# Performance work log

Measured on AMD Instinct MI355X. Metric: run time of the kernel, lower is better.

The kernel has to match this reference:

```python
import jax, jax.numpy as jnp
import numpy as np

IDIM = 256
N_UNITS = 512
N_LAYERS = 4
E_UNITS = 2048
H = 8
D_K = N_UNITS // H
EPS = 1e-5


def _layer_norm(x, g, b):
    mu = jnp.mean(x, axis=-1, keepdims=True)
    var = jnp.mean(jnp.square(x - mu), axis=-1, keepdims=True)
    return (x - mu) * jax.lax.rsqrt(var + EPS) * g + b


def setup_inputs() -> dict:
    key = jax.random.key(0)
    ks = jax.random.split(key, 16)
    s = 0.02
    inp = {
        'x': jax.random.normal(ks[0], (4, 2, 1024, IDIM), dtype=jnp.float32),
        'Win': jax.random.normal(ks[1], (N_UNITS, IDIM), dtype=jnp.float32) * s,
        'bin_': jnp.zeros((N_UNITS,), jnp.float32),
        'ln1_g': jnp.ones((N_LAYERS, N_UNITS), jnp.float32),
        'ln1_b': jnp.zeros((N_LAYERS, N_UNITS), jnp.float32),
        'Wq': jax.random.normal(ks[2], (N_LAYERS, N_UNITS, N_UNITS), dtype=jnp.float32) * s,
        'bq': jnp.zeros((N_LAYERS, N_UNITS), jnp.float32),
        'Wk': jax.random.normal(ks[3], (N_LAYERS, N_UNITS, N_UNITS), dtype=jnp.float32) * s,
        'bk': jnp.zeros((N_LAYERS, N_UNITS), jnp.float32),
        'Wv': jax.random.normal(ks[4], (N_LAYERS, N_UNITS, N_UNITS), dtype=jnp.float32) * s,
        'bv': jnp.zeros((N_LAYERS, N_UNITS), jnp.float32),
        'Wo': jax.random.normal(ks[5], (N_LAYERS, N_UNITS, N_UNITS), dtype=jnp.float32) * s,
        'bo': jnp.zeros((N_LAYERS, N_UNITS), jnp.float32),
        'ln2_g': jnp.ones((N_LAYERS, N_UNITS), jnp.float32),
        'ln2_b': jnp.zeros((N_LAYERS, N_UNITS), jnp.float32),
        'W1': jax.random.normal(ks[6], (N_LAYERS, E_UNITS, N_UNITS), dtype=jnp.float32) * s,
        'b1': jnp.zeros((N_LAYERS, E_UNITS), jnp.float32),
        'W2': jax.random.normal(ks[7], (N_LAYERS, N_UNITS, E_UNITS), dtype=jnp.float32) * s,
        'b2': jnp.zeros((N_LAYERS, N_UNITS), jnp.float32),
        'lno_g': jnp.ones((N_UNITS,), jnp.float32),
        'lno_b': jnp.zeros((N_UNITS,), jnp.float32),
    }
    return inp


def reference(x, Win, bin_, ln1_g, ln1_b, Wq, bq, Wk, bk, Wv, bv, Wo, bo,
              ln2_g, ln2_b, W1, b1, W2, b2, lno_g, lno_b):
    bs, num, T, dim = x.shape
    B = bs * num
    # input projection; e is kept as [B*T, n_units] like the torch code
    e = x.reshape(B * T, dim) @ Win.T + bin_
    scale = 1.0 / np.sqrt(D_K).astype(np.float32)
    for i in range(N_LAYERS):
        e = _layer_norm(e, ln1_g[i], ln1_b[i])
        # multi-head self-attention (dropout is identity in eval)
        q = (e @ Wq[i].T + bq[i]).reshape(B, T, H, D_K)
        k = (e @ Wk[i].T + bk[i]).reshape(B, T, H, D_K)
        v = (e @ Wv[i].T + bv[i]).reshape(B, T, H, D_K)
        scores = jnp.einsum('bthd,bshd->bhts', q, k) * scale  # [B,H,T,T]
        att = jax.nn.softmax(scores, axis=-1)
        ctx = jnp.einsum('bhts,bshd->bthd', att, v).reshape(B * T, N_UNITS)
        s = ctx @ Wo[i].T + bo[i]
        e = e + s
        e = _layer_norm(e, ln2_g[i], ln2_b[i])
        # position-wise feed-forward
        hdn = jnp.maximum(e @ W1[i].T + b1[i], 0.0)
        e = e + (hdn @ W2[i].T + b2[i])
    out = _layer_norm(e, lno_g, lno_b)
    return out.reshape(bs, num, T, N_UNITS)
```

## Files before the change

### kernel.cpp

```cpp
#include <hip/hip_runtime.h>
#include <hip/hip_bf16.h>
#include <math.h>
#include <stdint.h>

#define IDIM   256
#define NU     512
#define NL     4
#define EU     2048
#define NH     8
#define DK     64
#define TT     1024
#define NB     8
#define MTOT   8192

typedef short  bf16x8 __attribute__((ext_vector_type(8)));
typedef float  f32x4  __attribute__((ext_vector_type(4)));
typedef unsigned short ushortv2 __attribute__((ext_vector_type(2)));

__device__ __forceinline__ unsigned short f2b(float x) {
  unsigned int u = __float_as_uint(x);
  u += 0x7fffu + ((u >> 16) & 1u);
  return (unsigned short)(u >> 16);
}

__device__ __forceinline__ void gload16(const unsigned short* g, unsigned short* l) {
  auto gp = reinterpret_cast<const __attribute__((address_space(1))) unsigned int*>(
      reinterpret_cast<uintptr_t>(g));
  auto lp = reinterpret_cast<__attribute__((address_space(3))) unsigned int*>(
      reinterpret_cast<uintptr_t>(l));
  __builtin_amdgcn_global_load_lds(gp, lp, 16, 0, 0);
}

__global__ __launch_bounds__(256) void cvt_bf16(
    const float* __restrict__ src, unsigned short* __restrict__ dst, int n) {
  int i = (blockIdx.x * 256 + threadIdx.x) * 8;
  if (i >= n) return;
  float4 a = *(const float4*)(src + i);
  float4 b = *(const float4*)(src + i + 4);
  bf16x8 r;
  r[0] = (short)f2b(a.x); r[1] = (short)f2b(a.y);
  r[2] = (short)f2b(a.z); r[3] = (short)f2b(a.w);
  r[4] = (short)f2b(b.x); r[5] = (short)f2b(b.y);
  r[6] = (short)f2b(b.z); r[7] = (short)f2b(b.w);
  *(bf16x8*)(dst + i) = r;
}

#define GEMM_STAGE(BUF, KK)                                                  \
  _Pragma("unroll") for (int ii = 0; ii < 2; ++ii) {                         \
    gload16(ag + (size_t)(ii * 64) * kdim + (KK), &As[BUF][ii * 2048 + wv * 512]); \
    gload16(bg + (size_t)(ii * 64) * kdim + (KK), &Bs[BUF][ii * 2048 + wv * 512]); \
  }

#define GEMM_CORE(K_, KBEG, KEND)                                            \
  __shared__ unsigned short As[2][128 * 32];                                 \
  __shared__ unsigned short Bs[2][128 * 32];                                 \
  const int kdim = (K_);                                                     \
  const int tid  = threadIdx.x;                                              \
  const int lane = tid & 63;                                                 \
  const int wv   = tid >> 6;                                                 \
  const int wm   = (wv >> 1) * 64;                                           \
  const int wn   = (wv & 1) * 64;                                            \
  const int fr   = lane & 15;                                                \
  const int fc   = lane >> 4;                                                \
  const int srow = wv * 16 + (lane >> 2);                                    \
  const int skk  = (lane & 3) * 8;                                           \
  const unsigned short* ag = A + (size_t)(m0 + srow) * kdim + skk;           \
  const unsigned short* bg = W + (size_t)(n0 + srow) * kdim + skk;           \
  f32x4 acc[4][4];                                                           \
  _Pragma("unroll") for (int i = 0; i < 4; ++i)                              \
    _Pragma("unroll") for (int j = 0; j < 4; ++j)                            \
      acc[i][j] = (f32x4){0.f, 0.f, 0.f, 0.f};                               \
  int cur = 0;                                                               \
  GEMM_STAGE(0, (KBEG))                                                      \
  for (int k0 = (KBEG); k0 < (KEND); k0 += 32) {                             \
    __syncthreads();   \
    if (k0 + 32 < (KEND)) { GEMM_STAGE(cur ^ 1, k0 + 32) }                   \
    const unsigned short* acu = As[cur];                                     \
    const unsigned short* bcu = Bs[cur];                                     \
    bf16x8 af[4], bfr[4];                                                    \
    _Pragma("unroll") for (int mi = 0; mi < 4; ++mi)                         \
      af[mi] = *(const bf16x8*)&acu[(wm + mi * 16 + fr) * 32 + fc * 8];      \
    _Pragma("unroll") for (int ni = 0; ni < 4; ++ni)                         \
      bfr[ni] = *(const bf16x8*)&bcu[(wn + ni * 16 + fr) * 32 + fc * 8];     \
    _Pragma("unroll") for (int mi = 0; mi < 4; ++mi)                         \
      _Pragma("unroll") for (int ni = 0; ni < 4; ++ni)                       \
        acc[mi][ni] = __builtin_amdgcn_mfma_f32_16x16x32_bf16(               \
            af[mi], bfr[ni], acc[mi][ni], 0, 0, 0);                          \
    cur ^= 1;                                                                \
  }

template<int MODE, bool RELU>
__global__ __launch_bounds__(256) void gemm_bf(
    const unsigned short* __restrict__ A, const unsigned short* __restrict__ W,
    const float* __restrict__ bias, float* __restrict__ Cf,
    unsigned short* __restrict__ Cb, int M, int N, int K, int kchunk) {
  const int m0 = blockIdx.y * 128;
  const int n0 = blockIdx.x * 128;
  const int kbeg = blockIdx.z * kchunk;
  const int kend = kbeg + kchunk;
  GEMM_CORE(K, kbeg, kend)

  const bool addb = (blockIdx.z == 0);
#pragma unroll
  for (int ni = 0; ni < 4; ++ni) {
    const int col = n0 + wn + ni * 16 + fr;
    const float bb = (MODE != 2 || addb) ? bias[col] : 0.f;
#pragma unroll
    for (int mi = 0; mi < 4; ++mi) {
      const int row = m0 + wm + mi * 16 + fc * 4;
#pragma unroll
      for (int j = 0; j < 4; ++j) {
        size_t off = (size_t)(row + j) * N + col;
        float r = acc[mi][ni][j] + bb;
        if (RELU) r = fmaxf(r, 0.f);
        if (MODE == 0) Cf[off] = r;
        else if (MODE == 1) Cb[off] = f2b(r);
        else atomicAdd(&Cf[off], r);
      }
    }
  }
}

__global__ __launch_bounds__(256) void gemm_qkv(
    const unsigned short* __restrict__ A,
    const unsigned short* __restrict__ Wq, const unsigned short* __restrict__ Wk,
    const unsigned short* __restrict__ Wv,
    const float* __restrict__ bq, const float* __restrict__ bk,
    const float* __restrict__ bv,
    unsigned short* __restrict__ Oq, unsigned short* __restrict__ Ok,
    unsigned short* __restrict__ Ov) {
  const int zz = blockIdx.z;
  const unsigned short* W  = zz == 0 ? Wq : (zz == 1 ? Wk : Wv);
  const float* bias        = zz == 0 ? bq : (zz == 1 ? bk : bv);
  unsigned short* C        = zz == 0 ? Oq : (zz == 1 ? Ok : Ov);
  const float scale        = zz == 0 ? 0.125f : 1.0f;
  const int m0 = blockIdx.y * 128;
  const int n0 = blockIdx.x * 128;
  GEMM_CORE(NU, 0, NU)

#pragma unroll
  for (int ni = 0; ni < 4; ++ni) {
    const int col = n0 + wn + ni * 16 + fr;
    const float bb = bias[col];
#pragma unroll
    for (int mi = 0; mi < 4; ++mi) {
      const int row = m0 + wm + mi * 16 + fc * 4;
#pragma unroll
      for (int j = 0; j < 4; ++j)
        C[(size_t)(row + j) * NU + col] = f2b((acc[mi][ni][j] + bb) * scale);
    }
  }
}

template<bool WB>
__global__ __launch_bounds__(256) void layernorm_inplace(
    float* __restrict__ e, const float* __restrict__ g,
    const float* __restrict__ b, unsigned short* __restrict__ eb) {
  const int row = blockIdx.x;
  float* x = e + (size_t)row * NU;
  const int tid = threadIdx.x;

  float2 v = *(const float2*)&x[tid * 2];
  float sum = v.x + v.y;
  float sq  = v.x * v.x + v.y * v.y;
#pragma unroll
  for (int o = 32; o > 0; o >>= 1) {
    sum += __shfl_down(sum, o);
    sq  += __shfl_down(sq, o);
  }
  __shared__ float ps[4], pq[4], stat[2];
  const int wid = tid >> 6, lane = tid & 63;
  if (lane == 0) { ps[wid] = sum; pq[wid] = sq; }
  __syncthreads();
  if (tid == 0) {
    float s = ps[0] + ps[1] + ps[2] + ps[3];
    float q = pq[0] + pq[1] + pq[2] + pq[3];
    float mu = s * (1.0f / NU);
    float var = q * (1.0f / NU) - mu * mu;
    stat[0] = mu;
    stat[1] = rsqrtf(var + 1e-5f);
  }
  __syncthreads();
  const float mu = stat[0], rstd = stat[1];
  const float2 gg = *(const float2*)&g[tid * 2];
  const float2 bb = *(const float2*)&b[tid * 2];
  v.x = (v.x - mu) * rstd * gg.x + bb.x;
  v.y = (v.y - mu) * rstd * gg.y + bb.y;
  *(float2*)&x[tid * 2] = v;
  if (WB) {
    ushortv2 o = {f2b(v.x), f2b(v.y)};
    *(ushortv2*)&eb[(size_t)row * NU + tid * 2] = o;
  }
}

__global__ __launch_bounds__(256) void flash_attn_mfma(
    const unsigned short* __restrict__ Q, const unsigned short* __restrict__ K,
    const unsigned short* __restrict__ V, unsigned short* __restrict__ O) {
  constexpr int LSTR = 72;
  constexpr int VSTR = 66;
  __shared__ unsigned short Ks[64 * LSTR];
  __shared__ unsigned short Vt[64 * VSTR];
  __shared__ unsigned short Ps[64 * LSTR];

  const int b = blockIdx.z, h = blockIdx.y;
  const int q0 = blockIdx.x * 64;
  const int tid = threadIdx.x;
  const int lane = tid & 63;
  const int w = tid >> 6;
  const int fr = lane & 15;
  const int fc = lane >> 4;

  const size_t hb = ((size_t)b * TT) * NU + h * DK;

  bf16x8 qf[2];
#pragma unroll
  for (int kc = 0; kc < 2; ++kc)
    qf[kc] = *(const bf16x8*)(Q + hb +
        (size_t)(q0 + w * 16 + fr) * NU + kc * 32 + fc * 8);

  f32x4 ctx[4];
#pragma unroll
  for (int ni = 0; ni < 4; ++ni) ctx[ni] = (f32x4){0.f, 0.f, 0.f, 0.f};
  float m_run[4], l_run[4];
#pragma unroll
  for (int j = 0; j < 4; ++j) { m_run[j] = -1e30f; l_run[j] = 0.f; }

  const int sr = tid >> 2;
  const int sd = (tid & 3) * 16;

  for (int kt = 0; kt < TT; kt += 64) {
    const unsigned short* kp = K + hb + (size_t)(kt + sr) * NU + sd;
    const unsigned short* vp = V + hb + (size_t)(kt + sr) * NU + sd;
    bf16x8 k0 = *(const bf16x8*)kp, k1 = *(const bf16x8*)(kp + 8);
    bf16x8 v0 = *(const bf16x8*)vp, v1 = *(const bf16x8*)(vp + 8);

    __syncthreads();
    *(bf16x8*)&Ks[sr * LSTR + sd]     = k0;
    *(bf16x8*)&Ks[sr * LSTR + sd + 8] = k1;
#pragma unroll
    for (int t = 0; t < 8; ++t) {
      Vt[(sd + t)     * VSTR + sr] = (unsigned short)v0[t];
      Vt[(sd + t + 8) * VSTR + sr] = (unsigned short)v1[t];
    }
    __syncthreads();

    bf16x8 kf[4][2];
#pragma unroll
    for (int ni = 0; ni < 4; ++ni)
#pragma unroll
      for (int kc = 0; kc < 2; ++kc)
        kf[ni][kc] = *(const bf16x8*)&Ks[(ni * 16 + fr) * LSTR + kc * 32 + fc * 8];

    f32x4 sacc[4];
#pragma unroll
    for (int ni = 0; ni < 4; ++ni) sacc[ni] = (f32x4){0.f, 0.f, 0.f, 0.f};
#pragma unroll
    for (int kc = 0; kc < 2; ++kc)
#pragma unroll
      for (int ni = 0; ni < 4; ++ni)
        sacc[ni] = __builtin_amdgcn_mfma_f32_16x16x32_bf16(
            qf[kc], kf[ni][kc], sacc[ni], 0, 0, 0);

    float cm[4];
#pragma unroll
    for (int j = 0; j < 4; ++j)
      cm[j] = fmaxf(fmaxf(sacc[0][j], sacc[1][j]),
                    fmaxf(sacc[2][j], sacc[3][j]));
#pragma unroll
    for (int mask = 1; mask < 16; mask <<= 1)
#pragma unroll
      for (int j = 0; j < 4; ++j)
        cm[j] = fmaxf(cm[j], __shfl_xor(cm[j], mask));

    int need = (cm[0] > m_run[0] + 8.f) | (cm[1] > m_run[1] + 8.f) |
               (cm[2] > m_run[2] + 8.f) | (cm[3] > m_run[3] + 8.f);
    if (__any(need)) {
#pragma unroll
      for (int j = 0; j < 4; ++j) {
        float mn = fmaxf(m_run[j], cm[j]);
        float corr = __expf(m_run[j] - mn);
        m_run[j] = mn;
        l_run[j] *= corr;
#pragma unroll
        for (int ni = 0; ni < 4; ++ni) ctx[ni][j] *= corr;
      }
    }
#pragma unroll
    for (int j = 0; j < 4; ++j)
#pragma unroll
      for (int ni = 0; ni < 4; ++ni) {
        float p = __expf(sacc[ni][j] - m_run[j]);
        l_run[j] += p;
        Ps[(w * 16 + fc * 4 + j) * LSTR + ni * 16 + fr] = f2b(p);
      }

    bf16x8 pf[2], vf[4][2];
#pragma unroll
    for (int kc = 0; kc < 2; ++kc)
      pf[kc] = *(const bf16x8*)&Ps[(w * 16 + fr) * LSTR + kc * 32 + fc * 8];
#pragma unroll
    for (int ni = 0; ni < 4; ++ni)
#pragma unroll
      for (int kc = 0; kc < 2; ++kc)
        vf[ni][kc] = *(const bf16x8*)&Vt[(ni * 16 + fr) * VSTR + kc * 32 + fc * 8];
#pragma unroll
    for (int kc = 0; kc < 2; ++kc)
#pragma unroll
      for (int ni = 0; ni < 4; ++ni)
        ctx[ni] = __builtin_amdgcn_mfma_f32_16x16x32_bf16(
            pf[kc], vf[ni][kc], ctx[ni], 0, 0, 0);
  }

#pragma unroll
  for (int j = 0; j < 4; ++j) {
    float l = l_run[j];
#pragma unroll
    for (int mask = 1; mask < 16; mask <<= 1)
      l += __shfl_xor(l, mask);
    const float inv = 1.0f / l;
    const int row = q0 + w * 16 + fc * 4 + j;
    unsigned short* dst = O + hb + (size_t)row * NU;
#pragma unroll
    for (int ni = 0; ni < 4; ++ni)
      dst[ni * 16 + fr] = f2b(ctx[ni][j] * inv);
  }
}

extern "C" void kernel_launch(void* const* d_in, const int* in_sizes, int n_in,
                              void* d_out, int out_size, void* d_ws, size_t ws_size,
                              hipStream_t stream) {
  const float* x     = (const float*)d_in[0];
  const float* Win   = (const float*)d_in[1];
  const float* bin_  = (const float*)d_in[2];
  const float* ln1_g = (const float*)d_in[3];
  const float* ln1_b = (const float*)d_in[4];
  const float* Wq    = (const float*)d_in[5];
  const float* bq    = (const float*)d_in[6];
  const float* Wk    = (const float*)d_in[7];
  const float* bk    = (const float*)d_in[8];
  const float* Wv    = (const float*)d_in[9];
  const float* bv    = (const float*)d_in[10];
  const float* Wo    = (const float*)d_in[11];
  const float* bo    = (const float*)d_in[12];
  const float* ln2_g = (const float*)d_in[13];
  const float* ln2_b = (const float*)d_in[14];
  const float* W1    = (const float*)d_in[15];
  const float* b1    = (const float*)d_in[16];
  const float* W2    = (const float*)d_in[17];
  const float* b2    = (const float*)d_in[18];
  const float* lno_g = (const float*)d_in[19];
  const float* lno_b = (const float*)d_in[20];

  float* e = (float*)d_out;
  unsigned short* wsb = (unsigned short*)d_ws;
  const size_t M1 = 1u << 20;
  unsigned short* q    = wsb;
  unsigned short* k    = wsb + 4 * M1;
  unsigned short* v    = wsb + 8 * M1;
  unsigned short* ctx  = wsb + 12 * M1;
  unsigned short* hdn  = wsb;
  unsigned short* xbf  = wsb + 4 * M1;
  unsigned short* winb = wsb + 6 * M1;
  unsigned short* ebf  = wsb + 16 * M1;
  unsigned short* wqb  = wsb + 20 * M1;
  unsigned short* wkb  = wsb + 21 * M1;
  unsigned short* wvb  = wsb + 22 * M1;
  unsigned short* wob  = wsb + 23 * M1;
  unsigned short* w1b  = wsb + 24 * M1;
  unsigned short* w2b  = wsb + 28 * M1;

  const dim3 blk(256);
  cvt_bf16<<<1024, blk, 0, stream>>>(x,   xbf,  MTOT * IDIM);
  cvt_bf16<<<64,   blk, 0, stream>>>(Win, winb, NU * IDIM);
  cvt_bf16<<<512,  blk, 0, stream>>>(Wq,  wqb,  NL * NU * NU);
  cvt_bf16<<<512,  blk, 0, stream>>>(Wk,  wkb,  NL * NU * NU);
  cvt_bf16<<<512,  blk, 0, stream>>>(Wv,  wvb,  NL * NU * NU);
  cvt_bf16<<<512,  blk, 0, stream>>>(Wo,  wob,  NL * NU * NU);
  cvt_bf16<<<2048, blk, 0, stream>>>(W1,  w1b,  NL * EU * NU);
  cvt_bf16<<<2048, blk, 0, stream>>>(W2,  w2b,  NL * NU * EU);

  const dim3 gProjIn(NU / 128, MTOT / 128);
  const dim3 gQKV(NU / 128, MTOT / 128, 3);
  const dim3 gWo(NU / 128, MTOT / 128, 4);
  const dim3 gF1(EU / 128, MTOT / 128);
  const dim3 gF2(NU / 128, MTOT / 128, 4);
  const dim3 gAttn(TT / 64, NH, NB);

  gemm_bf<0, false><<<gProjIn, blk, 0, stream>>>(
      xbf, winb, bin_, e, nullptr, MTOT, NU, IDIM, IDIM);

  for (int i = 0; i < NL; ++i) {
    layernorm_inplace<true><<<MTOT, blk, 0, stream>>>(e, ln1_g + i * NU, ln1_b + i * NU, ebf);

    gemm_qkv<<<gQKV, blk, 0, stream>>>(ebf, wqb + (size_t)i * NU * NU,
                                       wkb + (size_t)i * NU * NU,
                                       wvb + (size_t)i * NU * NU,
                                       bq + i * NU, bk + i * NU, bv + i * NU,
                                       q, k, v);

    flash_attn_mfma<<<gAttn, blk, 0, stream>>>(q, k, v, ctx);

    gemm_bf<2, false><<<gWo, blk, 0, stream>>>(
        ctx, wob + (size_t)i * NU * NU, bo + i * NU, e, nullptr,
        MTOT, NU, NU, NU / 4);

    layernorm_inplace<true><<<MTOT, blk, 0, stream>>>(e, ln2_g + i * NU, ln2_b + i * NU, ebf);

    gemm_bf<1, true><<<gF1, blk, 0, stream>>>(
        ebf, w1b + (size_t)i * EU * NU, b1 + i * EU, nullptr, hdn,
        MTOT, EU, NU, NU);

    gemm_bf<2, false><<<gF2, blk, 0, stream>>>(
        hdn, w2b + (size_t)i * NU * EU, b2 + i * NU, e, nullptr,
        MTOT, NU, EU, EU / 4);
  }

  layernorm_inplace<false><<<MTOT, blk, 0, stream>>>(e, lno_g, lno_b, nullptr);
}
```

Baseline: 1.212 ms.

## Transpose V in QKV epilogue, register-staged GEMM loads, wave-per-row layernorm, fused conversion

Several changes land at once. The QKV kernel now writes V pre-transposed, so flash attention loads V tiles with vector stores instead of scattered transposes into shared memory. The GEMM core replaces async global-to-LDS double buffering with register prefetch into a single padded LDS tile, which adds a second barrier per k-step. Layernorm uses one wave per row with no shared-memory reduction, the eight conversion launches become one kernel, and the split-K factor for Wo and FFN2 drops from 4 to 2, which means fewer atomics but less parallelism.

Result: faster. 982.6 us (-18.9%).

```diff
diff --git a/kernel.cpp b/kernel.cpp
--- a/kernel.cpp
+++ b/kernel.cpp
@@ -15,7 +15,8 @@
 
 typedef short  bf16x8 __attribute__((ext_vector_type(8)));
 typedef float  f32x4  __attribute__((ext_vector_type(4)));
-typedef unsigned short ushortv2 __attribute__((ext_vector_type(2)));
+typedef unsigned short ushort4v __attribute__((ext_vector_type(4)));
+typedef unsigned short ushort8v __attribute__((ext_vector_type(8)));
 
 __device__ __forceinline__ unsigned short f2b(float x) {
   unsigned int u = __float_as_uint(x);
@@ -23,37 +24,36 @@
   return (unsigned short)(u >> 16);
 }
 
-__device__ __forceinline__ void gload16(const unsigned short* g, unsigned short* l) {
-  auto gp = reinterpret_cast<const __attribute__((address_space(1))) unsigned int*>(
-      reinterpret_cast<uintptr_t>(g));
-  auto lp = reinterpret_cast<__attribute__((address_space(3))) unsigned int*>(
-      reinterpret_cast<uintptr_t>(l));
-  __builtin_amdgcn_global_load_lds(gp, lp, 16, 0, 0);
-}
-
-__global__ __launch_bounds__(256) void cvt_bf16(
-    const float* __restrict__ src, unsigned short* __restrict__ dst, int n) {
-  int i = (blockIdx.x * 256 + threadIdx.x) * 8;
-  if (i >= n) return;
-  float4 a = *(const float4*)(src + i);
-  float4 b = *(const float4*)(src + i + 4);
-  bf16x8 r;
-  r[0] = (short)f2b(a.x); r[1] = (short)f2b(a.y);
-  r[2] = (short)f2b(a.z); r[3] = (short)f2b(a.w);
-  r[4] = (short)f2b(b.x); r[5] = (short)f2b(b.y);
-  r[6] = (short)f2b(b.z); r[7] = (short)f2b(b.w);
-  *(bf16x8*)(dst + i) = r;
-}
-
-#define GEMM_STAGE(BUF, KK)                                                  \
-  _Pragma("unroll") for (int ii = 0; ii < 2; ++ii) {                         \
-    gload16(ag + (size_t)(ii * 64) * kdim + (KK), &As[BUF][ii * 2048 + wv * 512]); \
-    gload16(bg + (size_t)(ii * 64) * kdim + (KK), &Bs[BUF][ii * 2048 + wv * 512]); \
-  }
+__device__ __forceinline__ void cvt_seg(const float* s, unsigned short* d, int blk) {
+  int i = (blk * 256 + (int)threadIdx.x) * 8;
+  float4 a = *(const float4*)(s + i);
+  float4 b = *(const float4*)(s + i + 4);
+  ushort8v r = {f2b(a.x), f2b(a.y), f2b(a.z), f2b(a.w),
+                f2b(b.x), f2b(b.y), f2b(b.z), f2b(b.w)};
+  *(ushort8v*)(d + i) = r;
+}
+
+__global__ __launch_bounds__(256) void cvt_all(
+    const float* x, const float* Win, const float* Wq, const float* Wk,
+    const float* Wv, const float* Wo, const float* W1, const float* W2,
+    unsigned short* xb, unsigned short* winb, unsigned short* wqb,
+    unsigned short* wkb, unsigned short* wvb, unsigned short* wob,
+    unsigned short* w1b, unsigned short* w2b) {
+  int b = blockIdx.x;
+  if      (b < 1024) cvt_seg(x,   xb,   b);
+  else if (b < 1088) cvt_seg(Win, winb, b - 1024);
+  else if (b < 1600) cvt_seg(Wq,  wqb,  b - 1088);
+  else if (b < 2112) cvt_seg(Wk,  wkb,  b - 1600);
+  else if (b < 2624) cvt_seg(Wv,  wvb,  b - 2112);
+  else if (b < 3136) cvt_seg(Wo,  wob,  b - 2624);
+  else if (b < 5184) cvt_seg(W1,  w1b,  b - 3136);
+  else               cvt_seg(W2,  w2b,  b - 5184);
+}
 
 #define GEMM_CORE(K_, KBEG, KEND)                                            \
-  __shared__ unsigned short As[2][128 * 32];                                 \
-  __shared__ unsigned short Bs[2][128 * 32];                                 \
+  constexpr int LSTR = 40;                                                   \
+  __shared__ unsigned short As[128 * LSTR];                                  \
+  __shared__ unsigned short Bs[128 * LSTR];                                  \
   const int kdim = (K_);                                                     \
   const int tid  = threadIdx.x;                                              \
   const int lane = tid & 63;                                                 \
@@ -62,31 +62,41 @@
   const int wn   = (wv & 1) * 64;                                            \
   const int fr   = lane & 15;                                                \
   const int fc   = lane >> 4;                                                \
-  const int srow = wv * 16 + (lane >> 2);                                    \
-  const int skk  = (lane & 3) * 8;                                           \
-  const unsigned short* ag = A + (size_t)(m0 + srow) * kdim + skk;           \
-  const unsigned short* bg = W + (size_t)(n0 + srow) * kdim + skk;           \
+  const int sr   = tid >> 1;                                                 \
+  const int sh   = (tid & 1) * 16;                                           \
+  const short* aptr = (const short*)A + (size_t)(m0 + sr) * kdim + sh;       \
+  const short* wptr = (const short*)W + (size_t)(n0 + sr) * kdim + sh;       \
+  short* asd = (short*)&As[sr * LSTR + sh];                                  \
+  short* bsd = (short*)&Bs[sr * LSTR + sh];                                  \
   f32x4 acc[4][4];                                                           \
   _Pragma("unroll") for (int i = 0; i < 4; ++i)                              \
     _Pragma("unroll") for (int j = 0; j < 4; ++j)                            \
       acc[i][j] = (f32x4){0.f, 0.f, 0.f, 0.f};                               \
-  int cur = 0;                                                               \
-  GEMM_STAGE(0, (KBEG))                                                      \
+  bf16x8 pa0 = *(const bf16x8*)(aptr + (KBEG));                              \
+  bf16x8 pa1 = *(const bf16x8*)(aptr + (KBEG) + 8);                          \
+  bf16x8 pb0 = *(const bf16x8*)(wptr + (KBEG));                              \
+  bf16x8 pb1 = *(const bf16x8*)(wptr + (KBEG) + 8);                          \
   for (int k0 = (KBEG); k0 < (KEND); k0 += 32) {                             \
-    __syncthreads();   \
-    if (k0 + 32 < (KEND)) { GEMM_STAGE(cur ^ 1, k0 + 32) }                   \
-    const unsigned short* acu = As[cur];                                     \
-    const unsigned short* bcu = Bs[cur];                                     \
+    __syncthreads();                                                         \
+    *(bf16x8*)asd = pa0;  *(bf16x8*)(asd + 8) = pa1;                         \
+    *(bf16x8*)bsd = pb0;  *(bf16x8*)(bsd + 8) = pb1;                         \
+    __syncthreads();                                                         \
+    const int kn = k0 + 32;                                                  \
+    if (kn < (KEND)) {                                                       \
+      pa0 = *(const bf16x8*)(aptr + kn);                                     \
+      pa1 = *(const bf16x8*)(aptr + kn + 8);                                 \
+      pb0 = *(const bf16x8*)(wptr + kn);                                     \
+      pb1 = *(const bf16x8*)(wptr + kn + 8);                                 \
+    }                                                                        \
     bf16x8 af[4], bfr[4];                                                    \
     _Pragma("unroll") for (int mi = 0; mi < 4; ++mi)                         \
-      af[mi] = *(const bf16x8*)&acu[(wm + mi * 16 + fr) * 32 + fc * 8];      \
+      af[mi] = *(const bf16x8*)&As[(wm + mi * 16 + fr) * LSTR + fc * 8];     \
     _Pragma("unroll") for (int ni = 0; ni < 4; ++ni)                         \
-      bfr[ni] = *(const bf16x8*)&bcu[(wn + ni * 16 + fr) * 32 + fc * 8];     \
+      bfr[ni] = *(const bf16x8*)&Bs[(wn + ni * 16 + fr) * LSTR + fc * 8];    \
     _Pragma("unroll") for (int mi = 0; mi < 4; ++mi)                         \
       _Pragma("unroll") for (int ni = 0; ni < 4; ++ni)                       \
         acc[mi][ni] = __builtin_amdgcn_mfma_f32_16x16x32_bf16(               \
             af[mi], bfr[ni], acc[mi][ni], 0, 0, 0);                          \
-    cur ^= 1;                                                                \
   }
 
 template<int MODE, bool RELU>
@@ -128,78 +138,95 @@
     const float* __restrict__ bq, const float* __restrict__ bk,
     const float* __restrict__ bv,
     unsigned short* __restrict__ Oq, unsigned short* __restrict__ Ok,
-    unsigned short* __restrict__ Ov) {
+    unsigned short* __restrict__ Ovt) {
   const int zz = blockIdx.z;
   const unsigned short* W  = zz == 0 ? Wq : (zz == 1 ? Wk : Wv);
   const float* bias        = zz == 0 ? bq : (zz == 1 ? bk : bv);
-  unsigned short* C        = zz == 0 ? Oq : (zz == 1 ? Ok : Ov);
   const float scale        = zz == 0 ? 0.125f : 1.0f;
   const int m0 = blockIdx.y * 128;
   const int n0 = blockIdx.x * 128;
   GEMM_CORE(NU, 0, NU)
 
-#pragma unroll
-  for (int ni = 0; ni < 4; ++ni) {
-    const int col = n0 + wn + ni * 16 + fr;
-    const float bb = bias[col];
-#pragma unroll
-    for (int mi = 0; mi < 4; ++mi) {
-      const int row = m0 + wm + mi * 16 + fc * 4;
-#pragma unroll
-      for (int j = 0; j < 4; ++j)
-        C[(size_t)(row + j) * NU + col] = f2b((acc[mi][ni][j] + bb) * scale);
+  if (zz < 2) {
+    unsigned short* C = zz == 0 ? Oq : Ok;
+#pragma unroll
+    for (int ni = 0; ni < 4; ++ni) {
+      const int col = n0 + wn + ni * 16 + fr;
+      const float bb = bias[col];
+#pragma unroll
+      for (int mi = 0; mi < 4; ++mi) {
+        const int row = m0 + wm + mi * 16 + fc * 4;
+#pragma unroll
+        for (int j = 0; j < 4; ++j)
+          C[(size_t)(row + j) * NU + col] = f2b((acc[mi][ni][j] + bb) * scale);
+      }
     }
+  } else {
+#pragma unroll
+    for (int ni = 0; ni < 4; ++ni) {
+      const int col = n0 + wn + ni * 16 + fr;
+      const float bb = bias[col];
+      const int h = col >> 6, d = col & 63;
+#pragma unroll
+      for (int mi = 0; mi < 4; ++mi) {
+        const int row = m0 + wm + mi * 16 + fc * 4;
+        const int bi = row >> 10, t = row & 1023;
+        ushort4v o = {f2b(acc[mi][ni][0] + bb), f2b(acc[mi][ni][1] + bb),
+                      f2b(acc[mi][ni][2] + bb), f2b(acc[mi][ni][3] + bb)};
+        *(ushort4v*)&Ovt[(size_t)(((bi * NH + h) * DK) + d) * TT + t] = o;
+      }
+    }
   }
 }
 
 template<bool WB>
-__global__ __launch_bounds__(256) void layernorm_inplace(
+__global__ __launch_bounds__(256) void layernorm_wave(
     float* __restrict__ e, const float* __restrict__ g,
     const float* __restrict__ b, unsigned short* __restrict__ eb) {
-  const int row = blockIdx.x;
-  float* x = e + (size_t)row * NU;
-  const int tid = threadIdx.x;
-
-  float2 v = *(const float2*)&x[tid * 2];
-  float sum = v.x + v.y;
-  float sq  = v.x * v.x + v.y * v.y;
+  const int lane = threadIdx.x & 63;
+  const int row = blockIdx.x * 4 + (threadIdx.x >> 6);
+  float* x = e + (size_t)row * NU + lane * 8;
+
+  float4 v0 = *(const float4*)x;
+  float4 v1 = *(const float4*)(x + 4);
+  float sum = v0.x + v0.y + v0.z + v0.w + v1.x + v1.y + v1.z + v1.w;
+  float sq  = v0.x*v0.x + v0.y*v0.y + v0.z*v0.z + v0.w*v0.w +
+              v1.x*v1.x + v1.y*v1.y + v1.z*v1.z + v1.w*v1.w;
 #pragma unroll
   for (int o = 32; o > 0; o >>= 1) {
-    sum += __shfl_down(sum, o);
-    sq  += __shfl_down(sq, o);
-  }
-  __shared__ float ps[4], pq[4], stat[2];
-  const int wid = tid >> 6, lane = tid & 63;
-  if (lane == 0) { ps[wid] = sum; pq[wid] = sq; }
-  __syncthreads();
-  if (tid == 0) {
-    float s = ps[0] + ps[1] + ps[2] + ps[3];
-    float q = pq[0] + pq[1] + pq[2] + pq[3];
-    float mu = s * (1.0f / NU);
-    float var = q * (1.0f / NU) - mu * mu;
-    stat[0] = mu;
-    stat[1] = rsqrtf(var + 1e-5f);
-  }
-  __syncthreads();
-  const float mu = stat[0], rstd = stat[1];
-  const float2 gg = *(const float2*)&g[tid * 2];
-  const float2 bb = *(const float2*)&b[tid * 2];
-  v.x = (v.x - mu) * rstd * gg.x + bb.x;
-  v.y = (v.y - mu) * rstd * gg.y + bb.y;
-  *(float2*)&x[tid * 2] = v;
+    sum += __shfl_xor(sum, o);
+    sq  += __shfl_xor(sq, o);
+  }
+  const float mu = sum * (1.0f / NU);
+  const float rstd = rsqrtf(sq * (1.0f / NU) - mu * mu + 1e-5f);
+
+  const float4 g0 = *(const float4*)&g[lane * 8];
+  const float4 g1 = *(const float4*)&g[lane * 8 + 4];
+  const float4 b0 = *(const float4*)&b[lane * 8];
+  const float4 b1 = *(const float4*)&b[lane * 8 + 4];
+  v0.x = (v0.x - mu) * rstd * g0.x + b0.x;
+  v0.y = (v0.y - mu) * rstd * g0.y + b0.y;
+  v0.z = (v0.z - mu) * rstd * g0.z + b0.z;
+  v0.w = (v0.w - mu) * rstd * g0.w + b0.w;
+  v1.x = (v1.x - mu) * rstd * g1.x + b1.x;
+  v1.y = (v1.y - mu) * rstd * g1.y + b1.y;
+  v1.z = (v1.z - mu) * rstd * g1.z + b1.z;
+  v1.w = (v1.w - mu) * rstd * g1.w + b1.w;
+  *(float4*)x = v0;
+  *(float4*)(x + 4) = v1;
   if (WB) {
-    ushortv2 o = {f2b(v.x), f2b(v.y)};
-    *(ushortv2*)&eb[(size_t)row * NU + tid * 2] = o;
+    ushort8v o = {f2b(v0.x), f2b(v0.y), f2b(v0.z), f2b(v0.w),
+                  f2b(v1.x), f2b(v1.y), f2b(v1.z), f2b(v1.w)};
+    *(ushort8v*)&eb[(size_t)row * NU + lane * 8] = o;
   }
 }
 
 __global__ __launch_bounds__(256) void flash_attn_mfma(
     const unsigned short* __restrict__ Q, const unsigned short* __restrict__ K,
-    const unsigned short* __restrict__ V, unsigned short* __restrict__ O) {
+    const unsigned short* __restrict__ VT, unsigned short* __restrict__ O) {
   constexpr int LSTR = 72;
-  constexpr int VSTR = 66;
   __shared__ unsigned short Ks[64 * LSTR];
-  __shared__ unsigned short Vt[64 * VSTR];
+  __shared__ unsigned short Vt[64 * LSTR];
   __shared__ unsigned short Ps[64 * LSTR];
 
   const int b = blockIdx.z, h = blockIdx.y;
@@ -211,6 +238,7 @@
   const int fc = lane >> 4;
 
   const size_t hb = ((size_t)b * TT) * NU + h * DK;
+  const size_t vb = ((size_t)(b * NH + h)) * DK * TT;
 
   bf16x8 qf[2];
 #pragma unroll
@@ -230,18 +258,15 @@
 
   for (int kt = 0; kt < TT; kt += 64) {
     const unsigned short* kp = K + hb + (size_t)(kt + sr) * NU + sd;
-    const unsigned short* vp = V + hb + (size_t)(kt + sr) * NU + sd;
+    const unsigned short* vp = VT + vb + (size_t)sr * TT + kt + sd;
     bf16x8 k0 = *(const bf16x8*)kp, k1 = *(const bf16x8*)(kp + 8);
     bf16x8 v0 = *(const bf16x8*)vp, v1 = *(const bf16x8*)(vp + 8);
 
     __syncthreads();
     *(bf16x8*)&Ks[sr * LSTR + sd]     = k0;
     *(bf16x8*)&Ks[sr * LSTR + sd + 8] = k1;
-#pragma unroll
-    for (int t = 0; t < 8; ++t) {
-      Vt[(sd + t)     * VSTR + sr] = (unsigned short)v0[t];
-      Vt[(sd + t + 8) * VSTR + sr] = (unsigned short)v1[t];
-    }
+    *(bf16x8*)&Vt[sr * LSTR + sd]     = v0;
+    *(bf16x8*)&Vt[sr * LSTR + sd + 8] = v1;
     __syncthreads();
 
     bf16x8 kf[4][2];
@@ -302,7 +327,7 @@
     for (int ni = 0; ni < 4; ++ni)
 #pragma unroll
       for (int kc = 0; kc < 2; ++kc)
-        vf[ni][kc] = *(const bf16x8*)&Vt[(ni * 16 + fr) * VSTR + kc * 32 + fc * 8];
+        vf[ni][kc] = *(const bf16x8*)&Vt[(ni * 16 + fr) * LSTR + kc * 32 + fc * 8];
 #pragma unroll
     for (int kc = 0; kc < 2; ++kc)
 #pragma unroll
@@ -356,7 +381,7 @@
   const size_t M1 = 1u << 20;
   unsigned short* q    = wsb;
   unsigned short* k    = wsb + 4 * M1;
-  unsigned short* v    = wsb + 8 * M1;
+  unsigned short* vT   = wsb + 8 * M1;
   unsigned short* ctx  = wsb + 12 * M1;
   unsigned short* hdn  = wsb;
   unsigned short* xbf  = wsb + 4 * M1;
@@ -370,41 +395,36 @@
   unsigned short* w2b  = wsb + 28 * M1;
 
   const dim3 blk(256);
-  cvt_bf16<<<1024, blk, 0, stream>>>(x,   xbf,  MTOT * IDIM);
-  cvt_bf16<<<64,   blk, 0, stream>>>(Win, winb, NU * IDIM);
-  cvt_bf16<<<512,  blk, 0, stream>>>(Wq,  wqb,  NL * NU * NU);
-  cvt_bf16<<<512,  blk, 0, stream>>>(Wk,  wkb,  NL * NU * NU);
-  cvt_bf16<<<512,  blk, 0, stream>>>(Wv,  wvb,  NL * NU * NU);
-  cvt_bf16<<<512,  blk, 0, stream>>>(Wo,  wob,  NL * NU * NU);
-  cvt_bf16<<<2048, blk, 0, stream>>>(W1,  w1b,  NL * EU * NU);
-  cvt_bf16<<<2048, blk, 0, stream>>>(W2,  w2b,  NL * NU * EU);
+  cvt_all<<<7232, blk, 0, stream>>>(x, Win, Wq, Wk, Wv, Wo, W1, W2,
+                                    xbf, winb, wqb, wkb, wvb, wob, w1b, w2b);
 
   const dim3 gProjIn(NU / 128, MTOT / 128);
   const dim3 gQKV(NU / 128, MTOT / 128, 3);
-  const dim3 gWo(NU / 128, MTOT / 128, 4);
+  const dim3 gWo(NU / 128, MTOT / 128, 2);
   const dim3 gF1(EU / 128, MTOT / 128);
-  const dim3 gF2(NU / 128, MTOT / 128, 4);
+  const dim3 gF2(NU / 128, MTOT / 128, 2);
   const dim3 gAttn(TT / 64, NH, NB);
+  const dim3 gLN(MTOT / 4);
 
   gemm_bf<0, false><<<gProjIn, blk, 0, stream>>>(
       xbf, winb, bin_, e, nullptr, MTOT, NU, IDIM, IDIM);
 
   for (int i = 0; i < NL; ++i) {
-    layernorm_inplace<true><<<MTOT, blk, 0, stream>>>(e, ln1_g + i * NU, ln1_b + i * NU, ebf);
+    layernorm_wave<true><<<gLN, blk, 0, stream>>>(e, ln1_g + i * NU, ln1_b + i * NU, ebf);
 
     gemm_qkv<<<gQKV, blk, 0, stream>>>(ebf, wqb + (size_t)i * NU * NU,
                                        wkb + (size_t)i * NU * NU,
                                        wvb + (size_t)i * NU * NU,
                                        bq + i * NU, bk + i * NU, bv + i * NU,
-                                       q, k, v);
-
-    flash_attn_mfma<<<gAttn, blk, 0, stream>>>(q, k, v, ctx);
+                                       q, k, vT);
+
+    flash_attn_mfma<<<gAttn, blk, 0, stream>>>(q, k, vT, ctx);
 
     gemm_bf<2, false><<<gWo, blk, 0, stream>>>(
         ctx, wob + (size_t)i * NU * NU, bo + i * NU, e, nullptr,
-        MTOT, NU, NU, NU / 4);
-
-    layernorm_inplace<true><<<MTOT, blk, 0, stream>>>(e, ln2_g + i * NU, ln2_b + i * NU, ebf);
+        MTOT, NU, NU, NU / 2);
+
+    layernorm_wave<true><<<gLN, blk, 0, stream>>>(e, ln2_g + i * NU, ln2_b + i * NU, ebf);
 
     gemm_bf<1, true><<<gF1, blk, 0, stream>>>(
         ebf, w1b + (size_t)i * EU * NU, b1 + i * EU, nullptr, hdn,
@@ -412,8 +432,8 @@
 
     gemm_bf<2, false><<<gF2, blk, 0, stream>>>(
         hdn, w2b + (size_t)i * NU * EU, b2 + i * NU, e, nullptr,
-        MTOT, NU, EU, EU / 4);
-  }
-
-  layernorm_inplace<false><<<MTOT, blk, 0, stream>>>(e, lno_g, lno_b, nullptr);
-}
+        MTOT, NU, EU, EU / 2);
+  }
+
+  layernorm_wave<false><<<gLN, blk, 0, stream>>>(e, lno_g, lno_b, nullptr);
+}
```
